# Kernel tuning notes

Hardware: AMD Instinct MI355X
Metric: run time of the kernel (lower is better)

## Reference

```python
import jax, jax.numpy as jnp
import numpy as np

HEADS = 8
HEAD_DIM = 64


def setup_inputs() -> dict:
    key = jax.random.key(0)
    ks = jax.random.split(key, 6)
    B, NQ, NC, D = 4, 1024, 8192, 512
    inner = HEADS * HEAD_DIM  # 512
    return {
        "x": jax.random.normal(ks[0], (B, NQ, D), dtype=jnp.float32),
        "context": jax.random.normal(ks[1], (B, NC, D), dtype=jnp.float32),
        "Wq": jax.random.normal(ks[2], (D, inner), dtype=jnp.float32) * (D ** -0.5),
        "Wkv": jax.random.normal(ks[3], (D, 2 * inner), dtype=jnp.float32) * (D ** -0.5),
        "Wout": jax.random.normal(ks[4], (inner, D), dtype=jnp.float32) * (inner ** -0.5),
        "bout": jax.random.normal(ks[5], (D,), dtype=jnp.float32) * 0.02,
    }


def reference(x, context, Wq, Wkv, Wout, bout):
    h, d = HEADS, HEAD_DIM
    scale = d ** -0.5
    b, nq, _ = x.shape
    nc = context.shape[1]
    q = x @ Wq                       # [b, nq, h*d]
    kv = context @ Wkv               # [b, nc, 2*h*d]
    k, v = jnp.split(kv, 2, axis=-1)
    # b n (h d) -> b h n d
    q = q.reshape(b, nq, h, d).transpose(0, 2, 1, 3)
    k = k.reshape(b, nc, h, d).transpose(0, 2, 1, 3)
    v = v.reshape(b, nc, h, d).transpose(0, 2, 1, 3)
    sim = jnp.einsum('bhid,bhjd->bhij', q, k) * scale  # [b, h, nq, nc]
    attn = jax.nn.softmax(sim, axis=-1)
    out = jnp.einsum('bhij,bhjd->bhid', attn, v)       # [b, h, nq, d]
    out = out.transpose(0, 2, 1, 3).reshape(b, nq, h * d)
    out = out @ Wout + bout          # [b, nq, queries_dim]
    return out.astype(x.dtype)
```

## Files before the change

### kernel.cpp

```cpp
#include <hip/hip_runtime.h>

#define B_   4
#define NQ_  1024
#define NC_  8192
#define D_   512
#define H_   8
#define HD_  64
#define NSPLIT 4
#define NCS  (NC_ / NSPLIT)

typedef __attribute__((ext_vector_type(4))) float f32x4;
typedef __attribute__((ext_vector_type(8))) short s16x8;
typedef __attribute__((ext_vector_type(4))) unsigned short u16x4;

__device__ inline unsigned short f2bf(float f) {
  unsigned int u = __float_as_uint(f);
  u += 0x7fffu + ((u >> 16) & 1u);
  return (unsigned short)(u >> 16);
}

#define GLL16(g, l)                                                            \
  __builtin_amdgcn_global_load_lds(                                            \
      (const __attribute__((address_space(1))) void*)(g),                      \
      (__attribute__((address_space(3))) void*)(l), 16, 0, 0)

__global__ void cvt_bf16(const float* __restrict__ in,
                         unsigned short* __restrict__ out, int n4) {
  int idx = blockIdx.x * blockDim.x + threadIdx.x;
  int stride = gridDim.x * blockDim.x;
  for (int i = idx; i < n4; i += stride) {
    float4 v = ((const float4*)in)[i];
    u16x4 o;
    o.x = f2bf(v.x); o.y = f2bf(v.y); o.z = f2bf(v.z); o.w = f2bf(v.w);
    *(u16x4*)&out[(long)i * 4] = o;
  }
}

__global__ void cvt_wT(const float* __restrict__ in,
                       unsigned short* __restrict__ out,
                       int K, int N, float scale) {
  int idx = blockIdx.x * 256 + threadIdx.x;
  if (idx < K * N) {
    int nn = idx / K, kk = idx - nn * K;
    out[idx] = f2bf(in[(long)kk * N + nn] * scale);
  }
}

template <int BM, int F32OUT>
__global__ __launch_bounds__(256, BM == 128 ? 2 : 4)
void gemm_bt(const unsigned short* __restrict__ A,
             const unsigned short* __restrict__ BT,
             void* __restrict__ C, const float* __restrict__ bias,
             int M, int N, int K) {
  constexpr int MR = BM / 32;
  __shared__ unsigned short As[BM * 32];
  __shared__ unsigned short Bs[BM * 32];
  const int tid = threadIdx.x;
  const int wid = tid >> 6;
  const int lane = tid & 63;
  const int l15 = lane & 15, l4 = lane >> 4;
  const int wr = wid >> 1, wc = wid & 1;
  const long brow = (long)blockIdx.y * BM;
  const long bcol = (long)blockIdx.x * BM;
  f32x4 acc[MR][MR] = {};

  for (int k0 = 0; k0 < K; k0 += 32) {
#pragma unroll
    for (int i = 0; i < BM / 64; ++i) {
      int c = i * 256 + tid;
      const unsigned short* ga = A  + (brow + (c >> 2)) * (long)K + k0 + (c & 3) * 8;
      const unsigned short* gb = BT + (bcol + (c >> 2)) * (long)K + k0 + (c & 3) * 8;
      GLL16(ga, (char*)As + i * 4096 + wid * 1024);
      GLL16(gb, (char*)Bs + i * 4096 + wid * 1024);
    }
    __syncthreads();
    s16x8 af[MR], bf[MR];
#pragma unroll
    for (int mi = 0; mi < MR; ++mi)
      af[mi] = *(const s16x8*)&As[(wr * (BM / 2) + mi * 16 + l15) * 32 + l4 * 8];
#pragma unroll
    for (int ni = 0; ni < MR; ++ni)
      bf[ni] = *(const s16x8*)&Bs[(wc * (BM / 2) + ni * 16 + l15) * 32 + l4 * 8];
#pragma unroll
    for (int mi = 0; mi < MR; ++mi)
#pragma unroll
      for (int ni = 0; ni < MR; ++ni)
        acc[mi][ni] = __builtin_amdgcn_mfma_f32_16x16x32_bf16(
            af[mi], bf[ni], acc[mi][ni], 0, 0, 0);
    __syncthreads();
  }

#pragma unroll
  for (int ni = 0; ni < MR; ++ni) {
    const long col = bcol + wc * (BM / 2) + ni * 16 + l15;
    float bv = 0.f;
    if (F32OUT) bv = bias[col];
#pragma unroll
    for (int mi = 0; mi < MR; ++mi) {
      const long row0 = brow + wr * (BM / 2) + mi * 16 + l4 * 4;
#pragma unroll
      for (int r = 0; r < 4; ++r) {
        float v = acc[mi][ni][r];
        if (F32OUT) ((float*)C)[(row0 + r) * N + col] = v + bv;
        else        ((unsigned short*)C)[(row0 + r) * N + col] = f2bf(v);
      }
    }
  }
}

__global__ __launch_bounds__(256, 2)
void vtrans(const unsigned short* __restrict__ kv,
            unsigned short* __restrict__ vt) {
  __shared__ unsigned short T[64 * 72];
  const int tid = threadIdx.x;
  const int bh = blockIdx.y, b = bh >> 3, h = bh & 7;
  const int nc0 = blockIdx.x * 64;
#pragma unroll
  for (int i = 0; i < 2; ++i) {
    int c = i * 256 + tid;
    int nc = c >> 3, dc = c & 7;
    s16x8 v = *(const s16x8*)&kv[((long)(b * NC_ + nc0 + nc)) * 1024 + 512 + h * 64 + dc * 8];
#pragma unroll
    for (int j = 0; j < 8; ++j)
      T[(dc * 8 + j) * 72 + nc] = (unsigned short)v[j];
  }
  __syncthreads();
#pragma unroll
  for (int i = 0; i < 2; ++i) {
    int c = i * 256 + tid;
    int d = c >> 3, ncc = c & 7;
    s16x8 t = *(const s16x8*)&T[d * 72 + ncc * 8];
    *(s16x8*)&vt[((long)(bh * 64 + d)) * NC_ + nc0 + ncc * 8] = t;
  }
}

__global__ __launch_bounds__(256, 6)
void attn_fwd(const unsigned short* __restrict__ q,
              const unsigned short* __restrict__ kv,
              const unsigned short* __restrict__ vt,
              float* __restrict__ Op, float* __restrict__ lp) {
  __shared__ unsigned short Ks[64 * 64];
  __shared__ unsigned short Vs[64 * 64];
  __shared__ unsigned short Ps[64 * 72];
  const int tid = threadIdx.x;
  const int wid = tid >> 6;
  const int lane = tid & 63;
  const int l15 = lane & 15, l4 = lane >> 4;
  const int bh = blockIdx.y, b = bh >> 3, h = bh & 7;
  const int q0 = blockIdx.x * 64;
  const int z = blockIdx.z;

  s16x8 qf[2];
  {
    const unsigned short* qrow =
        q + ((long)(b * NQ_ + q0 + wid * 16 + l15)) * 512 + h * 64;
#pragma unroll
    for (int ks = 0; ks < 2; ++ks)
      qf[ks] = *(const s16x8*)&qrow[ks * 32 + l4 * 8];
  }

  float lrun[4] = {0.f, 0.f, 0.f, 0.f};
  f32x4 o[4] = {};

  for (int it = 0; it < NCS / 64; ++it) {
    const int nc0 = z * NCS + it * 64;
#pragma unroll
    for (int i = 0; i < 2; ++i) {
      int c = i * 256 + tid;
      int row = c >> 3;
      int colb = ((c & 7) * 16) ^ ((row & 7) << 4);
      const unsigned short* gk = kv + ((long)(b * NC_ + nc0 + row)) * 1024 + h * 64 + (colb >> 1);
      const unsigned short* gv = vt + ((long)(bh * 64 + row)) * NC_ + nc0 + (colb >> 1);
      GLL16(gk, (char*)Ks + i * 4096 + wid * 1024);
      GLL16(gv, (char*)Vs + i * 4096 + wid * 1024);
    }
    __syncthreads();

    f32x4 s[4] = {};
#pragma unroll
    for (int ks = 0; ks < 2; ++ks) {
#pragma unroll
      for (int ni = 0; ni < 4; ++ni) {
        int kvc = ni * 16 + l15;
        s16x8 kf = *(const s16x8*)((const char*)Ks + (kvc << 7) +
                                   (((ks * 64 + l4 * 16)) ^ ((kvc & 7) << 4)));
        s[ni] = __builtin_amdgcn_mfma_f32_16x16x32_bf16(qf[ks], kf, s[ni], 0, 0, 0);
      }
    }

    float psum[4] = {0.f, 0.f, 0.f, 0.f};
#pragma unroll
    for (int ni = 0; ni < 4; ++ni) {
#pragma unroll
      for (int r = 0; r < 4; ++r) {
        float p = __builtin_amdgcn_exp2f(s[ni][r] * 1.44269504f);
        psum[r] += p;
        Ps[(wid * 16 + l4 * 4 + r) * 72 + ni * 16 + l15] = f2bf(p);
      }
    }
#pragma unroll
    for (int r = 0; r < 4; ++r) lrun[r] += psum[r];
    asm volatile("" ::: "memory");

#pragma unroll
    for (int ks = 0; ks < 2; ++ks) {
      s16x8 pa = *(const s16x8*)&Ps[(wid * 16 + l15) * 72 + ks * 32 + l4 * 8];
#pragma unroll
      for (int dn = 0; dn < 4; ++dn) {
        int d = dn * 16 + l15;
        s16x8 vf = *(const s16x8*)((const char*)Vs + (d << 7) +
                                   (((ks * 64 + l4 * 16)) ^ ((d & 7) << 4)));
        o[dn] = __builtin_amdgcn_mfma_f32_16x16x32_bf16(pa, vf, o[dn], 0, 0, 0);
      }
    }
    __syncthreads();
  }

#pragma unroll
  for (int r = 0; r < 4; ++r) {
    float l0 = lrun[r];
#pragma unroll
    for (int mk = 1; mk < 16; mk <<= 1)
      l0 += __shfl_xor(l0, mk, 64);
    if (l15 == 0)
      lp[((long)(z * 32 + bh)) * 1024 + q0 + wid * 16 + l4 * 4 + r] = l0;
  }
#pragma unroll
  for (int dn = 0; dn < 4; ++dn)
#pragma unroll
    for (int r = 0; r < 4; ++r)
      Op[(((long)(z * 32 + bh)) * 1024 + q0 + wid * 16 + l4 * 4 + r) * 64 +
         dn * 16 + l15] = o[dn][r];
}

__global__ __launch_bounds__(256, 8)
void attn_combine(const float* __restrict__ Op, const float* __restrict__ lp,
                  unsigned short* __restrict__ att) {
  int idx = blockIdx.x * 256 + threadIdx.x;
  int col4 = idx & 127;
  int row = idx >> 7;
  int b = row >> 10, nq = row & 1023;
  int h = col4 >> 4, d4 = col4 & 15;
  float4 acc = {0.f, 0.f, 0.f, 0.f};
  float lsum = 0.f;
#pragma unroll
  for (int s = 0; s < NSPLIT; ++s) {
    const float4 v = *(const float4*)&Op[(((long)(s * 32 + b * 8 + h)) * 1024 + nq) * 64 + d4 * 4];
    acc.x += v.x; acc.y += v.y; acc.z += v.z; acc.w += v.w;
    lsum += lp[((long)(s * 32 + b * 8 + h)) * 1024 + nq];
  }
  float inv = 1.f / lsum;
  u16x4 o;
  o.x = f2bf(acc.x * inv); o.y = f2bf(acc.y * inv);
  o.z = f2bf(acc.z * inv); o.w = f2bf(acc.w * inv);
  *(u16x4*)&att[(long)row * 512 + col4 * 4] = o;
}

extern "C" void kernel_launch(void* const* d_in, const int* in_sizes, int n_in,
                              void* d_out, int out_size, void* d_ws, size_t ws_size,
                              hipStream_t stream) {
  (void)in_sizes; (void)n_in; (void)out_size; (void)ws_size;
  const float* x    = (const float*)d_in[0];
  const float* ctx  = (const float*)d_in[1];
  const float* Wq   = (const float*)d_in[2];
  const float* Wkv  = (const float*)d_in[3];
  const float* Wout = (const float*)d_in[4];
  const float* bout = (const float*)d_in[5];
  float* out = (float*)d_out;

  char* w = (char*)d_ws;
  unsigned short* x_bf   = (unsigned short*)w; w += (size_t)4096 * 512 * 2;
  unsigned short* ctx_bf = (unsigned short*)w; w += (size_t)32768 * 512 * 2;
  unsigned short* wqT    = (unsigned short*)w; w += (size_t)512 * 512 * 2;
  unsigned short* wkvT   = (unsigned short*)w; w += (size_t)1024 * 512 * 2;
  unsigned short* woutT  = (unsigned short*)w; w += (size_t)512 * 512 * 2;
  unsigned short* q_bf   = (unsigned short*)w; w += (size_t)4096 * 512 * 2;
  unsigned short* kv_bf  = (unsigned short*)w; w += (size_t)32768 * 1024 * 2;
  unsigned short* vt_bf  = (unsigned short*)w; w += (size_t)32 * 64 * NC_ * 2;
  unsigned short* att_bf = (unsigned short*)w; w += (size_t)4096 * 512 * 2;
  float* Opart = (float*)ctx_bf;
  float* lpart = (float*)x_bf;

  cvt_bf16<<<512,  256, 0, stream>>>(x,   x_bf,   4096 * 512 / 4);
  cvt_bf16<<<2048, 256, 0, stream>>>(ctx, ctx_bf, 32768 * 512 / 4);
  cvt_wT<<<1024, 256, 0, stream>>>(Wq,   wqT,   512, 512,  0.125f);
  cvt_wT<<<2048, 256, 0, stream>>>(Wkv,  wkvT,  512, 1024, 1.f);
  cvt_wT<<<1024, 256, 0, stream>>>(Wout, woutT, 512, 512,  1.f);

  gemm_bt<64, 0><<<dim3(8, 64),   256, 0, stream>>>(x_bf,   wqT,  q_bf,  nullptr, 4096,  512,  512);
  gemm_bt<128, 0><<<dim3(8, 256), 256, 0, stream>>>(ctx_bf, wkvT, kv_bf, nullptr, 32768, 1024, 512);
  vtrans<<<dim3(128, 32), 256, 0, stream>>>(kv_bf, vt_bf);
  attn_fwd<<<dim3(16, 32, NSPLIT), 256, 0, stream>>>(q_bf, kv_bf, vt_bf, Opart, lpart);
  attn_combine<<<2048, 256, 0, stream>>>(Opart, lpart, att_bf);
  gemm_bt<64, 1><<<dim3(8, 64), 256, 0, stream>>>(att_bf, woutT, out, bout, 4096, 512, 512);
}
```

Measured before the change: 345.4 us.

## Keep attention probabilities in registers via transposed S MFMA and bpermute

Computes S transposed by swapping the MFMA operands, so each lane holds probabilities for one query row. The P tile for the PV MFMA is then built with packed bf16 conversion and ds_bpermute cross-lane shuffles, which removes the P shared-memory buffer and its store/load round trip. The log2(e) factor is folded into the Wq scale so the per-element multiply before exp2 goes away, and the row-sum reduction shrinks to two shuffles. This adds bpermute traffic and selects in the inner loop, and the lane mapping has to be exactly right.

```diff
diff --git a/kernel.cpp b/kernel.cpp
--- a/kernel.cpp
+++ b/kernel.cpp
@@ -141,7 +141,6 @@
               float* __restrict__ Op, float* __restrict__ lp) {
   __shared__ unsigned short Ks[64 * 64];
   __shared__ unsigned short Vs[64 * 64];
-  __shared__ unsigned short Ps[64 * 72];
   const int tid = threadIdx.x;
   const int wid = tid >> 6;
   const int lane = tid & 63;
@@ -159,7 +158,11 @@
       qf[ks] = *(const s16x8*)&qrow[ks * 32 + l4 * 8];
   }
 
-  float lrun[4] = {0.f, 0.f, 0.f, 0.f};
+  const int alo = (l15 + ((l4 & 1) << 5)) << 2;
+  const int ahi = alo + 64;
+  const int sel = l4 >> 1;
+
+  float lrun = 0.f;
   f32x4 o[4] = {};
 
   for (int it = 0; it < NCS / 64; ++it) {
@@ -176,7 +179,7 @@
     }
     __syncthreads();
 
-    f32x4 s[4] = {};
+    f32x4 st[4] = {};
 #pragma unroll
     for (int ks = 0; ks < 2; ++ks) {
 #pragma unroll
@@ -184,27 +187,44 @@
         int kvc = ni * 16 + l15;
         s16x8 kf = *(const s16x8*)((const char*)Ks + (kvc << 7) +
                                    (((ks * 64 + l4 * 16)) ^ ((kvc & 7) << 4)));
-        s[ni] = __builtin_amdgcn_mfma_f32_16x16x32_bf16(qf[ks], kf, s[ni], 0, 0, 0);
-      }
-    }
-
-    float psum[4] = {0.f, 0.f, 0.f, 0.f};
-#pragma unroll
-    for (int ni = 0; ni < 4; ++ni) {
+        st[ni] = __builtin_amdgcn_mfma_f32_16x16x32_bf16(kf, qf[ks], st[ni], 0, 0, 0);
+      }
+    }
+
+    float p[4][4];
+    float psum = 0.f;
+#pragma unroll
+    for (int ni = 0; ni < 4; ++ni)
 #pragma unroll
       for (int r = 0; r < 4; ++r) {
-        float p = __builtin_amdgcn_exp2f(s[ni][r] * 1.44269504f);
-        psum[r] += p;
-        Ps[(wid * 16 + l4 * 4 + r) * 72 + ni * 16 + l15] = f2bf(p);
-      }
-    }
-#pragma unroll
-    for (int r = 0; r < 4; ++r) lrun[r] += psum[r];
-    asm volatile("" ::: "memory");
+        float v = __builtin_amdgcn_exp2f(st[ni][r]);
+        p[ni][r] = v;
+        psum += v;
+      }
+    lrun += psum;
+
+    int pk[4][2];
+#pragma unroll
+    for (int ni = 0; ni < 4; ++ni)
+#pragma unroll
+      for (int u = 0; u < 2; ++u)
+        asm("v_cvt_pk_bf16_f32 %0, %1, %2"
+            : "=v"(pk[ni][u]) : "v"(p[ni][2 * u]), "v"(p[ni][2 * u + 1]));
 
 #pragma unroll
     for (int ks = 0; ks < 2; ++ks) {
-      s16x8 pa = *(const s16x8*)&Ps[(wid * 16 + l15) * 72 + ks * 32 + l4 * 8];
+      int pw[4];
+#pragma unroll
+      for (int u = 0; u < 2; ++u) {
+        int a0 = __builtin_amdgcn_ds_bpermute(alo, pk[2 * ks][u]);
+        int b0 = __builtin_amdgcn_ds_bpermute(alo, pk[2 * ks + 1][u]);
+        pw[u] = sel ? b0 : a0;
+        int a1 = __builtin_amdgcn_ds_bpermute(ahi, pk[2 * ks][u]);
+        int b1 = __builtin_amdgcn_ds_bpermute(ahi, pk[2 * ks + 1][u]);
+        pw[2 + u] = sel ? b1 : a1;
+      }
+      s16x8 pa;
+      __builtin_memcpy(&pa, pw, 16);
 #pragma unroll
       for (int dn = 0; dn < 4; ++dn) {
         int d = dn * 16 + l15;
@@ -216,14 +236,12 @@
     __syncthreads();
   }
 
-#pragma unroll
-  for (int r = 0; r < 4; ++r) {
-    float l0 = lrun[r];
-#pragma unroll
-    for (int mk = 1; mk < 16; mk <<= 1)
-      l0 += __shfl_xor(l0, mk, 64);
-    if (l15 == 0)
-      lp[((long)(z * 32 + bh)) * 1024 + q0 + wid * 16 + l4 * 4 + r] = l0;
+  {
+    float l0 = lrun;
+    l0 += __shfl_xor(l0, 16, 64);
+    l0 += __shfl_xor(l0, 32, 64);
+    if (lane < 16)
+      lp[((long)(z * 32 + bh)) * 1024 + q0 + wid * 16 + l15] = l0;
   }
 #pragma unroll
   for (int dn = 0; dn < 4; ++dn)
@@ -283,7 +301,7 @@
 
   cvt_bf16<<<512,  256, 0, stream>>>(x,   x_bf,   4096 * 512 / 4);
   cvt_bf16<<<2048, 256, 0, stream>>>(ctx, ctx_bf, 32768 * 512 / 4);
-  cvt_wT<<<1024, 256, 0, stream>>>(Wq,   wqT,   512, 512,  0.125f);
+  cvt_wT<<<1024, 256, 0, stream>>>(Wq,   wqT,   512, 512,  0.18033688f);
   cvt_wT<<<2048, 256, 0, stream>>>(Wkv,  wkvT,  512, 1024, 1.f);
   cvt_wT<<<1024, 256, 0, stream>>>(Wout, woutT, 512, 512,  1.f);
 
```

Result: no change. 349.0 us (+1.1%).
